# Performance work log

Measured on AMD Instinct MI355X. Metric: run time of the kernel, lower is better.

Reference implementation:

```python
import jax, jax.numpy as jnp
import numpy as np

EMBED_DIM = 1024
NUM_HEADS = 16
HEAD_DIM = EMBED_DIM // NUM_HEADS


def setup_inputs() -> dict:
    key = jax.random.key(0)
    ks = jax.random.split(key, 11)
    L, N, E = 2048, 4, EMBED_DIM
    s = 1.0 / np.sqrt(E)
    return {
        "query": jax.random.normal(ks[0], (L, N, E), jnp.float32),
        "key": jax.random.normal(ks[1], (L, N, E), jnp.float32),
        "value": jax.random.normal(ks[2], (L, N, E), jnp.float32),
        "Wq": jax.random.normal(ks[3], (E, E), jnp.float32) * s,
        "bq": jax.random.normal(ks[4], (E,), jnp.float32) * s,
        "Wk": jax.random.normal(ks[5], (E, E), jnp.float32) * s,
        "bk": jax.random.normal(ks[6], (E,), jnp.float32) * s,
        "Wv": jax.random.normal(ks[7], (E, E), jnp.float32) * s,
        "bv": jax.random.normal(ks[8], (E,), jnp.float32) * s,
        "Wo": jax.random.normal(ks[9], (E, E), jnp.float32) * s,
        "bo": jax.random.normal(ks[10], (E,), jnp.float32) * s,
    }


def reference(query, key, value, Wq, bq, Wk, bk, Wv, bv, Wo, bo):
    # query/key/value: [L, N, E] (seq-first, as in nn.MultiheadAttention)
    L, N, E = query.shape
    H, D = NUM_HEADS, HEAD_DIM
    scaling = float(D) ** -0.5

    # nn.Linear: x @ W.T + b
    q = (query @ Wq.T + bq) * scaling           # [L, N, E]
    k = key @ Wk.T + bk                          # [S, N, E]
    v = value @ Wv.T + bv                        # [S, N, E]

    S = k.shape[0]
    # [L, N, E] -> [N*H, L, D]
    q = q.reshape(L, N * H, D).transpose(1, 0, 2)
    k = k.reshape(S, N * H, D).transpose(1, 0, 2)
    v = v.reshape(S, N * H, D).transpose(1, 0, 2)

    # attention scores: [N*H, L, S]
    scores = jnp.einsum('bld,bsd->bls', q, k)
    attn = jax.nn.softmax(scores, axis=-1)       # dropout p=0.0 (eval)

    out = jnp.einsum('bls,bsd->bld', attn, v)    # [N*H, L, D]
    out = out.transpose(1, 0, 2).reshape(L, N, E)
    attn_output = out @ Wo.T + bo                # [L, N, E]

    # need_weights=True: average attention over heads -> [N, L, S]
    avg_weights = attn.reshape(N, H, L, S).sum(axis=1) / H
    return attn_output, avg_weights
```

## Files before the change

kernel.cpp:

```cpp
#include <hip/hip_runtime.h>
#include <stdint.h>


typedef __attribute__((ext_vector_type(8))) short bf16x8;
typedef __attribute__((ext_vector_type(4))) float f32x4;

#define MFMA(a, b, c) __builtin_amdgcn_mfma_f32_16x16x32_bf16((a), (b), (c), 0, 0, 0)

__device__ __forceinline__ ushort f2bf(float f) {
    uint32_t u = __builtin_bit_cast(uint32_t, f);
    u += 0x7fffu + ((u >> 16) & 1u);
    return (ushort)(u >> 16);
}

__global__ __launch_bounds__(256) void k_proj(
    const float* __restrict__ Xq, const float* __restrict__ Xk, const float* __restrict__ Xv,
    const float* __restrict__ Wq, const float* __restrict__ bq,
    const float* __restrict__ Wk, const float* __restrict__ bk,
    const float* __restrict__ Wv, const float* __restrict__ bv,
    ushort* __restrict__ Qa, ushort* __restrict__ Ka, ushort* __restrict__ Vt)
{
    const int z = blockIdx.z;
    const float* X = (z == 0) ? Xq : (z == 1) ? Xk : Xv;
    const float* W = (z == 0) ? Wq : (z == 1) ? Wk : Wv;
    const float* B = (z == 0) ? bq : (z == 1) ? bk : bv;

    __shared__ __align__(16) ushort xt[128][40];
    __shared__ __align__(16) ushort wt[128][40];

    const int t = threadIdx.x;
    const int lane = t & 63;
    const int w = t >> 6;
    const int wr = w >> 1, wc = w & 1;
    const int c = lane & 15, g = lane >> 4;

    const int xrow0 = blockIdx.x * 128;
    const int wrow0 = blockIdx.y * 128;

    f32x4 acc[4][4] = {};

    for (int kt = 0; kt < 32; ++kt) {
        const int k0 = kt * 32;
        __syncthreads();
#pragma unroll
        for (int i = 0; i < 4; ++i) {
            int slot = t + i * 256;
            int row = slot >> 3, seg = slot & 7;
            float4 xv4 = *(const float4*)(X + (size_t)(xrow0 + row) * 1024 + k0 + seg * 4);
            uint2 px;
            px.x = (uint)f2bf(xv4.x) | ((uint)f2bf(xv4.y) << 16);
            px.y = (uint)f2bf(xv4.z) | ((uint)f2bf(xv4.w) << 16);
            *(uint2*)&xt[row][seg * 4] = px;
            float4 wv4 = *(const float4*)(W + (size_t)(wrow0 + row) * 1024 + k0 + seg * 4);
            uint2 pw;
            pw.x = (uint)f2bf(wv4.x) | ((uint)f2bf(wv4.y) << 16);
            pw.y = (uint)f2bf(wv4.z) | ((uint)f2bf(wv4.w) << 16);
            *(uint2*)&wt[row][seg * 4] = pw;
        }
        __syncthreads();

        const ushort (*At)[40] = (z == 2) ? wt : xt;
        const ushort (*Bt)[40] = (z == 2) ? xt : wt;
        bf16x8 af[4], bfr[4];
#pragma unroll
        for (int m = 0; m < 4; ++m) af[m]  = *(const bf16x8*)&At[wr * 64 + m * 16 + c][g * 8];
#pragma unroll
        for (int n = 0; n < 4; ++n) bfr[n] = *(const bf16x8*)&Bt[wc * 64 + n * 16 + c][g * 8];
#pragma unroll
        for (int m = 0; m < 4; ++m)
#pragma unroll
            for (int n = 0; n < 4; ++n)
                acc[m][n] = MFMA(af[m], bfr[n], acc[m][n]);
    }

    const float QS = 0.125f * 1.44269504088896340736f;
#pragma unroll
    for (int m = 0; m < 4; ++m)
#pragma unroll
        for (int n = 0; n < 4; ++n)
#pragma unroll
            for (int i = 0; i < 4; ++i) {
                int rowi = ((z == 2) ? wrow0 : xrow0) + wr * 64 + m * 16 + 4 * g + i;
                int coli = ((z == 2) ? xrow0 : wrow0) + wc * 64 + n * 16 + c;
                int e = (z == 2) ? rowi : coli;
                int r = (z == 2) ? coli : rowi;
                float v = acc[m][n][i] + B[e];
                if (z == 0) v *= QS;
                ushort bv16 = f2bf(v);
                int nn = r & 3, l = r >> 2, h = e >> 6, d = e & 63;
                int bh = nn * 16 + h;
                if (z == 2) Vt[((size_t)bh * 64 + d) * 2048 + l] = bv16;
                else {
                    ushort* o = (z == 0) ? Qa : Ka;
                    o[((size_t)bh * 2048 + l) * 64 + d] = bv16;
                }
            }
}

__global__ __launch_bounds__(512) void k_attn(
    const ushort* __restrict__ Qa, const ushort* __restrict__ Ka, const ushort* __restrict__ Vt,
    ushort* __restrict__ ctx, float* __restrict__ mbuf, float* __restrict__ lbuf)
{
    __shared__ __align__(16) ushort kt[64][72];
    __shared__ __align__(16) ushort vt[64][72];
    __shared__ __align__(16) ushort pt[8][16][72];

    const int t = threadIdx.x;
    const int lane = t & 63;
    const int w = t >> 6;
    const int c = lane & 15, g = lane >> 4;
    const int bh = blockIdx.y;
    const int n = bh >> 4, h = bh & 15;
    const int l0 = blockIdx.x * 128;
    const int lrow = l0 + w * 16 + c;

    bf16x8 aq0 = *(const bf16x8*)(Qa + ((size_t)bh * 2048 + lrow) * 64 + g * 8);
    bf16x8 aq1 = *(const bf16x8*)(Qa + ((size_t)bh * 2048 + lrow) * 64 + 32 + g * 8);

    f32x4 O[4] = {};
    float mrow[4] = {-1e30f, -1e30f, -1e30f, -1e30f};
    float lpart[4] = {0.f, 0.f, 0.f, 0.f};

    for (int st = 0; st < 32; ++st) {
        __syncthreads();
        {
            int row = t >> 3, seg = t & 7;
            *(uint4*)&kt[row][seg * 8] =
                *(const uint4*)(Ka + ((size_t)bh * 2048 + st * 64 + row) * 64 + seg * 8);
            *(uint4*)&vt[row][seg * 8] =
                *(const uint4*)(Vt + ((size_t)bh * 64 + row) * 2048 + st * 64 + seg * 8);
        }
        __syncthreads();

        f32x4 s[4];
#pragma unroll
        for (int ct = 0; ct < 4; ++ct) {
            bf16x8 b0 = *(const bf16x8*)&kt[ct * 16 + c][g * 8];
            bf16x8 b1 = *(const bf16x8*)&kt[ct * 16 + c][32 + g * 8];
            f32x4 zf = {};
            zf = MFMA(aq0, b0, zf);
            s[ct] = MFMA(aq1, b1, zf);
        }

        float tm[4];
#pragma unroll
        for (int i = 0; i < 4; ++i)
            tm[i] = fmaxf(fmaxf(s[0][i], s[1][i]), fmaxf(s[2][i], s[3][i]));
#pragma unroll
        for (int i = 0; i < 4; ++i) {
            tm[i] = fmaxf(tm[i], __shfl_xor(tm[i], 1));
            tm[i] = fmaxf(tm[i], __shfl_xor(tm[i], 2));
            tm[i] = fmaxf(tm[i], __shfl_xor(tm[i], 4));
            tm[i] = fmaxf(tm[i], __shfl_xor(tm[i], 8));
        }
#pragma unroll
        for (int i = 0; i < 4; ++i) {
            float mn = fmaxf(mrow[i], tm[i]);
            float al = exp2f(mrow[i] - mn);
            mrow[i] = mn;
            lpart[i] *= al;
            O[0][i] *= al; O[1][i] *= al; O[2][i] *= al; O[3][i] *= al;
        }
#pragma unroll
        for (int ct = 0; ct < 4; ++ct)
#pragma unroll
            for (int i = 0; i < 4; ++i) {
                float p = exp2f(s[ct][i] - mrow[i]);
                lpart[i] += p;
                pt[w][4 * g + i][ct * 16 + c] = f2bf(p);
            }

        bf16x8 ap0 = *(const bf16x8*)&pt[w][c][g * 8];
        bf16x8 ap1 = *(const bf16x8*)&pt[w][c][32 + g * 8];
#pragma unroll
        for (int dt = 0; dt < 4; ++dt) {
            bf16x8 b0 = *(const bf16x8*)&vt[dt * 16 + c][g * 8];
            bf16x8 b1 = *(const bf16x8*)&vt[dt * 16 + c][32 + g * 8];
            O[dt] = MFMA(ap0, b0, O[dt]);
            O[dt] = MFMA(ap1, b1, O[dt]);
        }
    }

    float lr[4];
#pragma unroll
    for (int i = 0; i < 4; ++i) {
        float v = lpart[i];
        v += __shfl_xor(v, 1); v += __shfl_xor(v, 2);
        v += __shfl_xor(v, 4); v += __shfl_xor(v, 8);
        lr[i] = v;
    }
#pragma unroll
    for (int i = 0; i < 4; ++i) {
        float rl = 1.0f / lr[i];
        int l = l0 + w * 16 + 4 * g + i;
        size_t base = ((size_t)l * 4 + n) * 1024 + h * 64;
#pragma unroll
        for (int dt = 0; dt < 4; ++dt)
            ctx[base + dt * 16 + c] = f2bf(O[dt][i] * rl);
    }
    if (c == 0) {
#pragma unroll
        for (int i = 0; i < 4; ++i) {
            int l = l0 + w * 16 + 4 * g + i;
            mbuf[(size_t)bh * 2048 + l] = mrow[i];
            lbuf[(size_t)bh * 2048 + l] = lr[i];
        }
    }
}

__global__ __launch_bounds__(256) void k_oproj(
    const ushort* __restrict__ ctx, const float* __restrict__ Wo,
    const float* __restrict__ bo, float* __restrict__ out)
{
    __shared__ __align__(16) ushort xt[128][40];
    __shared__ __align__(16) ushort wt[128][40];

    const int t = threadIdx.x;
    const int lane = t & 63;
    const int w = t >> 6;
    const int wr = w >> 1, wc = w & 1;
    const int c = lane & 15, g = lane >> 4;

    const int r0 = blockIdx.x * 128;
    const int e0 = blockIdx.y * 128;

    f32x4 acc[4][4] = {};

    for (int kt = 0; kt < 32; ++kt) {
        const int k0 = kt * 32;
        __syncthreads();
#pragma unroll
        for (int i = 0; i < 2; ++i) {
            int slot = t + i * 256;
            int row = slot >> 2, seg = slot & 3;
            *(uint4*)&xt[row][seg * 8] =
                *(const uint4*)(ctx + (size_t)(r0 + row) * 1024 + k0 + seg * 8);
        }
#pragma unroll
        for (int i = 0; i < 4; ++i) {
            int slot = t + i * 256;
            int row = slot >> 3, seg = slot & 7;
            float4 wv4 = *(const float4*)(Wo + (size_t)(e0 + row) * 1024 + k0 + seg * 4);
            uint2 pw;
            pw.x = (uint)f2bf(wv4.x) | ((uint)f2bf(wv4.y) << 16);
            pw.y = (uint)f2bf(wv4.z) | ((uint)f2bf(wv4.w) << 16);
            *(uint2*)&wt[row][seg * 4] = pw;
        }
        __syncthreads();

        bf16x8 af[4], bfr[4];
#pragma unroll
        for (int m = 0; m < 4; ++m) af[m]  = *(const bf16x8*)&xt[wr * 64 + m * 16 + c][g * 8];
#pragma unroll
        for (int n = 0; n < 4; ++n) bfr[n] = *(const bf16x8*)&wt[wc * 64 + n * 16 + c][g * 8];
#pragma unroll
        for (int m = 0; m < 4; ++m)
#pragma unroll
            for (int n = 0; n < 4; ++n)
                acc[m][n] = MFMA(af[m], bfr[n], acc[m][n]);
    }

#pragma unroll
    for (int m = 0; m < 4; ++m)
#pragma unroll
        for (int n = 0; n < 4; ++n)
#pragma unroll
            for (int i = 0; i < 4; ++i) {
                int r = r0 + wr * 64 + m * 16 + 4 * g + i;
                int e = e0 + wc * 64 + n * 16 + c;
                out[(size_t)r * 1024 + e] = acc[m][n][i] + bo[e];
            }
}

__global__ __launch_bounds__(512) void k_avg(
    const ushort* __restrict__ Qa, const ushort* __restrict__ Ka,
    const float* __restrict__ mbuf, const float* __restrict__ lbuf,
    float* __restrict__ avg)
{
    __shared__ float ms[16][64];
    __shared__ float rs[16][64];

    const int t = threadIdx.x;
    const int lane = t & 63;
    const int w = t >> 6;
    const int wr = w >> 2, wc = w & 3;
    const int c = lane & 15, g = lane >> 4;
    const int n = blockIdx.z;
    const int l0 = blockIdx.y * 64;
    const int s0 = blockIdx.x * 512 + wc * 128;

    for (int idx = t; idx < 1024; idx += 512) {
        int hh = idx >> 6, row = idx & 63;
        ms[hh][row] = mbuf[(size_t)(n * 16 + hh) * 2048 + l0 + row];
        rs[hh][row] = 1.0f / (16.0f * lbuf[(size_t)(n * 16 + hh) * 2048 + l0 + row]);
    }
    __syncthreads();

    f32x4 acc[2][8] = {};

    for (int h = 0; h < 16; ++h) {
        const int bh = n * 16 + h;
        bf16x8 aq[2][2];
#pragma unroll
        for (int rt = 0; rt < 2; ++rt) {
            int row = l0 + wr * 32 + rt * 16 + c;
            aq[rt][0] = *(const bf16x8*)(Qa + ((size_t)bh * 2048 + row) * 64 + g * 8);
            aq[rt][1] = *(const bf16x8*)(Qa + ((size_t)bh * 2048 + row) * 64 + 32 + g * 8);
        }
        float mr[8], rl[8];
#pragma unroll
        for (int rt = 0; rt < 2; ++rt)
#pragma unroll
            for (int i = 0; i < 4; ++i) {
                mr[rt * 4 + i] = ms[h][wr * 32 + rt * 16 + 4 * g + i];
                rl[rt * 4 + i] = rs[h][wr * 32 + rt * 16 + 4 * g + i];
            }
#pragma unroll
        for (int ct = 0; ct < 8; ++ct) {
            int srow = s0 + ct * 16 + c;
            bf16x8 b0 = *(const bf16x8*)(Ka + ((size_t)bh * 2048 + srow) * 64 + g * 8);
            bf16x8 b1 = *(const bf16x8*)(Ka + ((size_t)bh * 2048 + srow) * 64 + 32 + g * 8);
#pragma unroll
            for (int rt = 0; rt < 2; ++rt) {
                f32x4 zf = {};
                zf = MFMA(aq[rt][0], b0, zf);
                zf = MFMA(aq[rt][1], b1, zf);
#pragma unroll
                for (int i = 0; i < 4; ++i)
                    acc[rt][ct][i] += exp2f(zf[i] - mr[rt * 4 + i]) * rl[rt * 4 + i];
            }
        }
    }

#pragma unroll
    for (int rt = 0; rt < 2; ++rt)
#pragma unroll
        for (int i = 0; i < 4; ++i) {
            int row = l0 + wr * 32 + rt * 16 + 4 * g + i;
#pragma unroll
            for (int ct = 0; ct < 8; ++ct)
                avg[((size_t)n * 2048 + row) * 2048 + s0 + ct * 16 + c] = acc[rt][ct][i];
        }
}

extern "C" void kernel_launch(void* const* d_in, const int* in_sizes, int n_in,
                              void* d_out, int out_size, void* d_ws, size_t ws_size,
                              hipStream_t stream)
{
    const float* query = (const float*)d_in[0];
    const float* key   = (const float*)d_in[1];
    const float* value = (const float*)d_in[2];
    const float* Wq = (const float*)d_in[3];
    const float* bq = (const float*)d_in[4];
    const float* Wk = (const float*)d_in[5];
    const float* bk = (const float*)d_in[6];
    const float* Wv = (const float*)d_in[7];
    const float* bv = (const float*)d_in[8];
    const float* Wo = (const float*)d_in[9];
    const float* bo = (const float*)d_in[10];

    float* out = (float*)d_out;
    float* avg = out + 8388608;

    ushort* Qa = (ushort*)d_ws;
    ushort* Ka = Qa + 8388608;
    float* mbuf = (float*)(Ka + 8388608);
    float* lbuf = mbuf + 131072;

    ushort* Vt  = (ushort*)avg;
    ushort* ctx = (ushort*)(out + 20971520);

    k_proj<<<dim3(64, 8, 3), 256, 0, stream>>>(query, key, value,
                                               Wq, bq, Wk, bk, Wv, bv,
                                               Qa, Ka, Vt);
    k_attn<<<dim3(16, 64), 512, 0, stream>>>(Qa, Ka, Vt, ctx, mbuf, lbuf);
    k_oproj<<<dim3(64, 8), 256, 0, stream>>>(ctx, Wo, bo, out);
    k_avg<<<dim3(4, 32, 4), 512, 0, stream>>>(Qa, Ka, mbuf, lbuf, avg);
}
```

Before: 710.2 us.

## Pre-convert inputs and weights to bf16; transpose attention MFMA for row-per-lane softmax

Adds a prep kernel that converts the query/key/value activations and all four weight matrices to bf16 once, stored in scratch space inside the output buffers. The projection GEMMs can then load bf16 tiles directly instead of converting fp32 on every tile reload, which halves their global traffic and drops the repeated conversion work. The attention kernel swaps the MFMA operand order so each lane owns one query row, removing most cross-lane max/sum shuffles, and packs P with v_cvt_pk_bf16_f32. The context output is staged through LDS so it is written coalesced. The cost is an extra kernel launch and a full fp32 read plus bf16 write pass over the inputs.

```diff
diff --git a/kernel.cpp b/kernel.cpp
--- a/kernel.cpp
+++ b/kernel.cpp
@@ -3,6 +3,7 @@
 
 
 typedef __attribute__((ext_vector_type(8))) short bf16x8;
+typedef __attribute__((ext_vector_type(4))) short s16x4;
 typedef __attribute__((ext_vector_type(4))) float f32x4;
 
 #define MFMA(a, b, c) __builtin_amdgcn_mfma_f32_16x16x32_bf16((a), (b), (c), 0, 0, 0)
@@ -13,16 +14,47 @@
     return (ushort)(u >> 16);
 }
 
+__global__ __launch_bounds__(256) void k_prep(
+    const float* __restrict__ xq, const float* __restrict__ xk, const float* __restrict__ xv,
+    const float* __restrict__ wq, const float* __restrict__ wk,
+    const float* __restrict__ wv, const float* __restrict__ wo,
+    ushort* __restrict__ xqb, ushort* __restrict__ xkb, ushort* __restrict__ xvb,
+    ushort* __restrict__ wqb, ushort* __restrict__ wkb,
+    ushort* __restrict__ wvb, ushort* __restrict__ wob)
+{
+    const int z = blockIdx.y;
+    const float* src; ushort* dst; int n8;
+    switch (z) {
+        case 0: src = xq; dst = xqb; n8 = 1048576; break;
+        case 1: src = xk; dst = xkb; n8 = 1048576; break;
+        case 2: src = xv; dst = xvb; n8 = 1048576; break;
+        case 3: src = wq; dst = wqb; n8 = 131072;  break;
+        case 4: src = wk; dst = wkb; n8 = 131072;  break;
+        case 5: src = wv; dst = wvb; n8 = 131072;  break;
+        default: src = wo; dst = wob; n8 = 131072; break;
+    }
+    int u = blockIdx.x * 256 + threadIdx.x;
+    if (u >= n8) return;
+    const float4* s4 = (const float4*)src;
+    float4 a = s4[2 * (size_t)u];
+    float4 b = s4[2 * (size_t)u + 1];
+    uint4 o;
+    o.x = (uint)f2bf(a.x) | ((uint)f2bf(a.y) << 16);
+    o.y = (uint)f2bf(a.z) | ((uint)f2bf(a.w) << 16);
+    o.z = (uint)f2bf(b.x) | ((uint)f2bf(b.y) << 16);
+    o.w = (uint)f2bf(b.z) | ((uint)f2bf(b.w) << 16);
+    *(uint4*)(dst + 8 * (size_t)u) = o;
+}
+
 __global__ __launch_bounds__(256) void k_proj(
-    const float* __restrict__ Xq, const float* __restrict__ Xk, const float* __restrict__ Xv,
-    const float* __restrict__ Wq, const float* __restrict__ bq,
-    const float* __restrict__ Wk, const float* __restrict__ bk,
-    const float* __restrict__ Wv, const float* __restrict__ bv,
+    const ushort* __restrict__ Xq, const ushort* __restrict__ Xk, const ushort* __restrict__ Xv,
+    const ushort* __restrict__ Wqb, const ushort* __restrict__ Wkb, const ushort* __restrict__ Wvb,
+    const float* __restrict__ bq, const float* __restrict__ bk, const float* __restrict__ bv,
     ushort* __restrict__ Qa, ushort* __restrict__ Ka, ushort* __restrict__ Vt)
 {
     const int z = blockIdx.z;
-    const float* X = (z == 0) ? Xq : (z == 1) ? Xk : Xv;
-    const float* W = (z == 0) ? Wq : (z == 1) ? Wk : Wv;
+    const ushort* X = (z == 0) ? Xq : (z == 1) ? Xk : Xv;
+    const ushort* W = (z == 0) ? Wqb : (z == 1) ? Wkb : Wvb;
     const float* B = (z == 0) ? bq : (z == 1) ? bk : bv;
 
     __shared__ __align__(16) ushort xt[128][40];
@@ -43,19 +75,13 @@
         const int k0 = kt * 32;
         __syncthreads();
 #pragma unroll
-        for (int i = 0; i < 4; ++i) {
+        for (int i = 0; i < 2; ++i) {
             int slot = t + i * 256;
-            int row = slot >> 3, seg = slot & 7;
-            float4 xv4 = *(const float4*)(X + (size_t)(xrow0 + row) * 1024 + k0 + seg * 4);
-            uint2 px;
-            px.x = (uint)f2bf(xv4.x) | ((uint)f2bf(xv4.y) << 16);
-            px.y = (uint)f2bf(xv4.z) | ((uint)f2bf(xv4.w) << 16);
-            *(uint2*)&xt[row][seg * 4] = px;
-            float4 wv4 = *(const float4*)(W + (size_t)(wrow0 + row) * 1024 + k0 + seg * 4);
-            uint2 pw;
-            pw.x = (uint)f2bf(wv4.x) | ((uint)f2bf(wv4.y) << 16);
-            pw.y = (uint)f2bf(wv4.z) | ((uint)f2bf(wv4.w) << 16);
-            *(uint2*)&wt[row][seg * 4] = pw;
+            int row = slot >> 2, seg = slot & 3;
+            *(uint4*)&xt[row][seg * 8] =
+                *(const uint4*)(X + (size_t)(xrow0 + row) * 1024 + k0 + seg * 8);
+            *(uint4*)&wt[row][seg * 8] =
+                *(const uint4*)(W + (size_t)(wrow0 + row) * 1024 + k0 + seg * 8);
         }
         __syncthreads();
 
@@ -101,14 +127,15 @@
     const ushort* __restrict__ Qa, const ushort* __restrict__ Ka, const ushort* __restrict__ Vt,
     ushort* __restrict__ ctx, float* __restrict__ mbuf, float* __restrict__ lbuf)
 {
-    __shared__ __align__(16) ushort kt[64][72];
-    __shared__ __align__(16) ushort vt[64][72];
-    __shared__ __align__(16) ushort pt[8][16][72];
+    __shared__ __align__(16) ushort smem[4608 * 2 + 8 * 16 * 72];
+    ushort (*kt)[72] = (ushort(*)[72])smem;
+    ushort (*vt)[72] = (ushort(*)[72])(smem + 4608);
 
     const int t = threadIdx.x;
     const int lane = t & 63;
     const int w = t >> 6;
     const int c = lane & 15, g = lane >> 4;
+    ushort* ptw = smem + 9216 + w * 1152;
     const int bh = blockIdx.y;
     const int n = bh >> 4, h = bh & 15;
     const int l0 = blockIdx.x * 128;
@@ -118,8 +145,7 @@
     bf16x8 aq1 = *(const bf16x8*)(Qa + ((size_t)bh * 2048 + lrow) * 64 + 32 + g * 8);
 
     f32x4 O[4] = {};
-    float mrow[4] = {-1e30f, -1e30f, -1e30f, -1e30f};
-    float lpart[4] = {0.f, 0.f, 0.f, 0.f};
+    float m = -1e30f, l = 0.f;
 
     for (int st = 0; st < 32; ++st) {
         __syncthreads();
@@ -132,84 +158,80 @@
         }
         __syncthreads();
 
-        f32x4 s[4];
+        f32x4 sc[4];
 #pragma unroll
         for (int ct = 0; ct < 4; ++ct) {
-            bf16x8 b0 = *(const bf16x8*)&kt[ct * 16 + c][g * 8];
-            bf16x8 b1 = *(const bf16x8*)&kt[ct * 16 + c][32 + g * 8];
-            f32x4 zf = {};
-            zf = MFMA(aq0, b0, zf);
-            s[ct] = MFMA(aq1, b1, zf);
-        }
-
-        float tm[4];
-#pragma unroll
-        for (int i = 0; i < 4; ++i)
-            tm[i] = fmaxf(fmaxf(s[0][i], s[1][i]), fmaxf(s[2][i], s[3][i]));
-#pragma unroll
-        for (int i = 0; i < 4; ++i) {
-            tm[i] = fmaxf(tm[i], __shfl_xor(tm[i], 1));
-            tm[i] = fmaxf(tm[i], __shfl_xor(tm[i], 2));
-            tm[i] = fmaxf(tm[i], __shfl_xor(tm[i], 4));
-            tm[i] = fmaxf(tm[i], __shfl_xor(tm[i], 8));
-        }
-#pragma unroll
-        for (int i = 0; i < 4; ++i) {
-            float mn = fmaxf(mrow[i], tm[i]);
-            float al = exp2f(mrow[i] - mn);
-            mrow[i] = mn;
-            lpart[i] *= al;
-            O[0][i] *= al; O[1][i] *= al; O[2][i] *= al; O[3][i] *= al;
-        }
-#pragma unroll
-        for (int ct = 0; ct < 4; ++ct)
-#pragma unroll
-            for (int i = 0; i < 4; ++i) {
-                float p = exp2f(s[ct][i] - mrow[i]);
-                lpart[i] += p;
-                pt[w][4 * g + i][ct * 16 + c] = f2bf(p);
-            }
-
-        bf16x8 ap0 = *(const bf16x8*)&pt[w][c][g * 8];
-        bf16x8 ap1 = *(const bf16x8*)&pt[w][c][32 + g * 8];
+            bf16x8 kb0 = *(const bf16x8*)&kt[ct * 16 + c][g * 8];
+            bf16x8 kb1 = *(const bf16x8*)&kt[ct * 16 + c][32 + g * 8];
+            f32x4 z = {};
+            z = MFMA(kb0, aq0, z);
+            sc[ct] = MFMA(kb1, aq1, z);
+        }
+
+        float pm = fmaxf(fmaxf(sc[0][0], sc[0][1]), fmaxf(sc[0][2], sc[0][3]));
+#pragma unroll
+        for (int ct = 1; ct < 4; ++ct)
+            pm = fmaxf(pm, fmaxf(fmaxf(sc[ct][0], sc[ct][1]), fmaxf(sc[ct][2], sc[ct][3])));
+        pm = fmaxf(pm, __shfl_xor(pm, 16));
+        pm = fmaxf(pm, __shfl_xor(pm, 32));
+
+        float mn = fmaxf(m, pm);
+        float al = exp2f(m - mn);
+        m = mn;
+        l *= al;
+        O[0] *= al; O[1] *= al; O[2] *= al; O[3] *= al;
+
+#pragma unroll
+        for (int ct = 0; ct < 4; ++ct) {
+            float p0 = exp2f(sc[ct][0] - m);
+            float p1 = exp2f(sc[ct][1] - m);
+            float p2 = exp2f(sc[ct][2] - m);
+            float p3 = exp2f(sc[ct][3] - m);
+            l += (p0 + p1) + (p2 + p3);
+            uint pa, pb;
+            asm("v_cvt_pk_bf16_f32 %0, %1, %2" : "=v"(pa) : "v"(p0), "v"(p1));
+            asm("v_cvt_pk_bf16_f32 %0, %1, %2" : "=v"(pb) : "v"(p2), "v"(p3));
+            uint64_t pk = (uint64_t)pa | ((uint64_t)pb << 32);
+            *(s16x4*)&ptw[c * 72 + ct * 16 + g * 4] = __builtin_bit_cast(s16x4, pk);
+        }
+
+        bf16x8 ap0 = *(const bf16x8*)&ptw[c * 72 + g * 8];
+        bf16x8 ap1 = *(const bf16x8*)&ptw[c * 72 + 32 + g * 8];
 #pragma unroll
         for (int dt = 0; dt < 4; ++dt) {
-            bf16x8 b0 = *(const bf16x8*)&vt[dt * 16 + c][g * 8];
-            bf16x8 b1 = *(const bf16x8*)&vt[dt * 16 + c][32 + g * 8];
-            O[dt] = MFMA(ap0, b0, O[dt]);
-            O[dt] = MFMA(ap1, b1, O[dt]);
-        }
-    }
-
-    float lr[4];
-#pragma unroll
-    for (int i = 0; i < 4; ++i) {
-        float v = lpart[i];
-        v += __shfl_xor(v, 1); v += __shfl_xor(v, 2);
-        v += __shfl_xor(v, 4); v += __shfl_xor(v, 8);
-        lr[i] = v;
-    }
-#pragma unroll
-    for (int i = 0; i < 4; ++i) {
-        float rl = 1.0f / lr[i];
-        int l = l0 + w * 16 + 4 * g + i;
-        size_t base = ((size_t)l * 4 + n) * 1024 + h * 64;
-#pragma unroll
-        for (int dt = 0; dt < 4; ++dt)
-            ctx[base + dt * 16 + c] = f2bf(O[dt][i] * rl);
-    }
-    if (c == 0) {
-#pragma unroll
-        for (int i = 0; i < 4; ++i) {
-            int l = l0 + w * 16 + 4 * g + i;
-            mbuf[(size_t)bh * 2048 + l] = mrow[i];
-            lbuf[(size_t)bh * 2048 + l] = lr[i];
-        }
+            bf16x8 vb0 = *(const bf16x8*)&vt[dt * 16 + c][g * 8];
+            bf16x8 vb1 = *(const bf16x8*)&vt[dt * 16 + c][32 + g * 8];
+            O[dt] = MFMA(vb0, ap0, O[dt]);
+            O[dt] = MFMA(vb1, ap1, O[dt]);
+        }
+    }
+
+    float lsum = l;
+    lsum += __shfl_xor(lsum, 16);
+    lsum += __shfl_xor(lsum, 32);
+    float rl = 1.0f / lsum;
+
+    __syncthreads();
+    float* otw = (float*)smem + w * 1040;
+#pragma unroll
+    for (int dt = 0; dt < 4; ++dt)
+#pragma unroll
+        for (int r = 0; r < 4; ++r)
+            otw[c * 65 + dt * 16 + 4 * g + r] = O[dt][r] * rl;
+#pragma unroll
+    for (int qq = 0; qq < 16; ++qq) {
+        float v = otw[qq * 65 + lane];
+        int lr2 = l0 + w * 16 + qq;
+        ctx[((size_t)lr2 * 4 + n) * 1024 + h * 64 + lane] = f2bf(v);
+    }
+    if (g == 0) {
+        mbuf[(size_t)bh * 2048 + l0 + w * 16 + c] = m;
+        lbuf[(size_t)bh * 2048 + l0 + w * 16 + c] = lsum;
     }
 }
 
 __global__ __launch_bounds__(256) void k_oproj(
-    const ushort* __restrict__ ctx, const float* __restrict__ Wo,
+    const ushort* __restrict__ ctx, const ushort* __restrict__ Wob,
     const float* __restrict__ bo, float* __restrict__ out)
 {
     __shared__ __align__(16) ushort xt[128][40];
@@ -235,16 +257,8 @@
             int row = slot >> 2, seg = slot & 3;
             *(uint4*)&xt[row][seg * 8] =
                 *(const uint4*)(ctx + (size_t)(r0 + row) * 1024 + k0 + seg * 8);
-        }
-#pragma unroll
-        for (int i = 0; i < 4; ++i) {
-            int slot = t + i * 256;
-            int row = slot >> 3, seg = slot & 7;
-            float4 wv4 = *(const float4*)(Wo + (size_t)(e0 + row) * 1024 + k0 + seg * 4);
-            uint2 pw;
-            pw.x = (uint)f2bf(wv4.x) | ((uint)f2bf(wv4.y) << 16);
-            pw.y = (uint)f2bf(wv4.z) | ((uint)f2bf(wv4.w) << 16);
-            *(uint2*)&wt[row][seg * 4] = pw;
+            *(uint4*)&wt[row][seg * 8] =
+                *(const uint4*)(Wob + (size_t)(e0 + row) * 1024 + k0 + seg * 8);
         }
         __syncthreads();
 
@@ -367,13 +381,23 @@
     float* mbuf = (float*)(Ka + 8388608);
     float* lbuf = mbuf + 131072;
 
-    ushort* Vt  = (ushort*)avg;
-    ushort* ctx = (ushort*)(out + 20971520);
-
-    k_proj<<<dim3(64, 8, 3), 256, 0, stream>>>(query, key, value,
-                                               Wq, bq, Wk, bk, Wv, bv,
-                                               Qa, Ka, Vt);
+    ushort* ob  = (ushort*)out;
+    ushort* av16 = (ushort*)avg;
+    ushort* Xbq = ob;
+    ushort* Xbk = ob + 8388608;
+    ushort* Vt  = av16;
+    ushort* Xbv = av16 + 8388608;
+    ushort* Wqb = av16 + 16777216;
+    ushort* Wkb = Wqb + 1048576;
+    ushort* Wvb = Wkb + 1048576;
+    ushort* Wob = Wvb + 1048576;
+    ushort* ctx = av16 + 25165824;
+
+    k_prep<<<dim3(4096, 7), 256, 0, stream>>>(query, key, value, Wq, Wk, Wv, Wo,
+                                              Xbq, Xbk, Xbv, Wqb, Wkb, Wvb, Wob);
+    k_proj<<<dim3(64, 8, 3), 256, 0, stream>>>(Xbq, Xbk, Xbv, Wqb, Wkb, Wvb,
+                                               bq, bk, bv, Qa, Ka, Vt);
     k_attn<<<dim3(16, 64), 512, 0, stream>>>(Qa, Ka, Vt, ctx, mbuf, lbuf);
-    k_oproj<<<dim3(64, 8), 256, 0, stream>>>(ctx, Wo, bo, out);
+    k_oproj<<<dim3(64, 8), 256, 0, stream>>>(ctx, Wob, bo, out);
     k_avg<<<dim3(4, 32, 4), 512, 0, stream>>>(Qa, Ka, mbuf, lbuf, avg);
 }
```

After: 620.9 us. 1.14x faster.
